# Performance work log

Hardware: AMD Instinct MI355X
Metric: run time of the kernel (lower is better)

The kernel has to match this reference:

```python
import jax, jax.numpy as jnp
import numpy as np

B, T, D, H, E, K = 2, 1024, 1024, 16, 8, 2
HD = D // H
EPS = 1e-5


def _layer_norm(x, g, b):
    m = jnp.mean(x, axis=-1, keepdims=True)
    v = jnp.mean(jnp.square(x - m), axis=-1, keepdims=True)
    return (x - m) * jax.lax.rsqrt(v + EPS) * g + b


def setup_inputs() -> dict:
    key = jax.random.key(0)
    ks = jax.random.split(key, 8)
    s = 0.02
    return {
        "key": jax.random.normal(ks[0], (B, T, D), jnp.float32),
        "ln0_g": jnp.ones((D,), jnp.float32),
        "ln0_b": jnp.zeros((D,), jnp.float32),
        "Wv": s * jax.random.normal(ks[1], (D, D), jnp.float32),
        "Wk": s * jax.random.normal(ks[2], (D, D), jnp.float32),
        "Wq": s * jax.random.normal(ks[3], (D, D), jnp.float32),
        "Wo": s * jax.random.normal(ks[4], (D, D), jnp.float32),
        "ln1_g": jnp.ones((D,), jnp.float32),
        "ln1_b": jnp.zeros((D,), jnp.float32),
        "Wg": s * jax.random.normal(ks[5], (D, E), jnp.float32),
        "bg": jnp.zeros((E,), jnp.float32),
        "W1": s * jax.random.normal(ks[6], (E, D, D), jnp.float32),
        "b1": jnp.zeros((E, D), jnp.float32),
        "W2": s * jax.random.normal(ks[7], (E, D, D), jnp.float32),
        "b2": jnp.zeros((E, D), jnp.float32),
    }


def reference(key, ln0_g, ln0_b, Wv, Wk, Wq, Wo, ln1_g, ln1_b, Wg, bg, W1, b1, W2, b2):
    # pre-norm (shared for q/k/v since query=value=None)
    kn = _layer_norm(key, ln0_g, ln0_b)
    v = (kn @ Wv).reshape(B, T, H, HD)
    k = (kn @ Wk).reshape(B, T, H, HD)
    q = (kn @ Wq).reshape(B, T, H, HD)
    energy = jnp.einsum('bqhd,bkhd->bhqk', q, k)
    # note: source scales by sqrt(input_dim), not sqrt(head_dim)
    attn = jax.nn.softmax(energy / jnp.sqrt(jnp.asarray(D, energy.dtype)), axis=-1)
    o = jnp.einsum('bhqk,bkhd->bqhd', attn, v).reshape(B, T, D) @ Wo
    a = o + key  # residual onto key (query is None)
    xn = _layer_norm(a, ln1_g, ln1_b)
    # --- MoE (top-2 gating, noise_std=0 -> deterministic) ---
    xf = xn.reshape(-1, D)  # [N, D]
    logits = xf @ Wg + bg  # [N, E]
    scores, idx = jax.lax.top_k(logits, K)  # [N, K]
    w = jax.nn.softmax(scores, axis=-1)  # K=2 -> softmax over top-k scores
    # dense dispatch-combine: combine[N,E] = scatter of top-k weights
    combine = jnp.sum(jax.nn.one_hot(idx, E, dtype=xf.dtype) * w[..., None], axis=1)
    h = jax.nn.gelu(jnp.einsum('nd,edh->neh', xf, W1) + b1, approximate=False)
    eo = jnp.einsum('neh,ehf->nef', h, W2) + b2
    moe = jnp.einsum('ne,nef->nf', combine, eo).reshape(B, T, D)
    return moe + a  # out_dim == input_dim -> residual
```

## Files before the change

kernel.cpp:

```cpp
#include <hip/hip_runtime.h>
#include <hip/hip_bf16.h>

#define N_TOK 2048
#define DMODEL 1024
#define NE 8
#define ND (N_TOK * DMODEL)
#define MAT (DMODEL * DMODEL)

typedef __hip_bfloat16 bf16;
typedef __attribute__((ext_vector_type(8))) short s16x8;
typedef __attribute__((ext_vector_type(4))) float f32x4;

__device__ __forceinline__ float b2f(bf16 x) { return __bfloat162float(x); }
__device__ __forceinline__ bf16 f2b(float x) { return __float2bfloat16(x); }

__device__ __forceinline__ bool flag_bf16(const void* ones) {
    return *(const unsigned int*)ones == 0x3F803F80u;
}
__device__ __forceinline__ float ldx(const void* p, size_t i, bool bf) {
    return bf ? __bfloat162float(((const bf16*)p)[i]) : ((const float*)p)[i];
}
__device__ __forceinline__ float gelu_exact(float x) {
    return 0.5f * x * (1.f + erff(x * 0.70710678118654752f));
}

#define GLD16(gp, lp)                                                  \
    __builtin_amdgcn_global_load_lds(                                  \
        (const __attribute__((address_space(1))) void*)(gp),           \
        (__attribute__((address_space(3))) void*)(lp), 16, 0, 0)

#define MFMA16(a, b, c) __builtin_amdgcn_mfma_f32_16x16x32_bf16(a, b, c, 0, 0, 0)

__global__ __launch_bounds__(256) void prep_wT(const void* __restrict__ W,
                                               bf16* __restrict__ o,
                                               const void* __restrict__ ones) {
    bool bf = flag_bf16(ones);
    size_t moff = (size_t)blockIdx.z * MAT;
    int k0 = blockIdx.y * 64, n0 = blockIdx.x * 64;
    __shared__ float t[64][65];
    int tid = threadIdx.x;
#pragma unroll
    for (int i = 0; i < 16; ++i) {
        int idx = tid + 256 * i;
        int r = idx >> 6, c = idx & 63;
        t[r][c] = ldx(W, moff + (size_t)(k0 + r) * DMODEL + n0 + c, bf);
    }
    __syncthreads();
#pragma unroll
    for (int i = 0; i < 16; ++i) {
        int idx = tid + 256 * i;
        int r = idx >> 6, c = idx & 63;
        o[moff + (size_t)(n0 + r) * DMODEL + k0 + c] = f2b(t[c][r]);
    }
}

__global__ __launch_bounds__(256) void prep_wT2(const void* __restrict__ W0,
                                                const void* __restrict__ W1p,
                                                const void* __restrict__ W2p,
                                                bf16* __restrict__ oh,
                                                bf16* __restrict__ ol,
                                                const void* __restrict__ ones) {
    bool bf = flag_bf16(ones);
    int z = blockIdx.z;
    const void* W = (z == 0) ? W0 : (z == 1) ? W1p : W2p;
    size_t moff = (size_t)z * MAT;
    int k0 = blockIdx.y * 64, n0 = blockIdx.x * 64;
    __shared__ float t[64][65];
    int tid = threadIdx.x;
#pragma unroll
    for (int i = 0; i < 16; ++i) {
        int idx = tid + 256 * i;
        int r = idx >> 6, c = idx & 63;
        t[r][c] = ldx(W, (size_t)(k0 + r) * DMODEL + n0 + c, bf);
    }
    __syncthreads();
#pragma unroll
    for (int i = 0; i < 16; ++i) {
        int idx = tid + 256 * i;
        int r = idx >> 6, c = idx & 63;
        float x = t[c][r];
        bf16 hi = f2b(x);
        size_t oi = moff + (size_t)(n0 + r) * DMODEL + k0 + c;
        oh[oi] = hi;
        ol[oi] = f2b(x - b2f(hi));
    }
}

__global__ __launch_bounds__(256) void ln_kernel(const void* __restrict__ in, int in_ext,
                                                 const void* __restrict__ g,
                                                 const void* __restrict__ bb,
                                                 float* __restrict__ out32,
                                                 bf16* __restrict__ outh,
                                                 bf16* __restrict__ outl,
                                                 const void* __restrict__ ones) {
    bool bf = flag_bf16(ones);
    bool inbf = in_ext && bf;
    int row = blockIdx.x, tid = threadIdx.x;
    int lane = tid & 63, wave = tid >> 6;
    float x[4];
#pragma unroll
    for (int i = 0; i < 4; ++i) {
        int idx = tid + 256 * i;
        x[i] = inbf ? b2f(((const bf16*)in)[(size_t)row * DMODEL + idx])
                    : ((const float*)in)[(size_t)row * DMODEL + idx];
    }
    float s = x[0] + x[1] + x[2] + x[3];
    float s2 = x[0] * x[0] + x[1] * x[1] + x[2] * x[2] + x[3] * x[3];
#pragma unroll
    for (int off = 32; off; off >>= 1) {
        s += __shfl_xor(s, off);
        s2 += __shfl_xor(s2, off);
    }
    __shared__ float red[8];
    if (lane == 0) { red[wave] = s; red[4 + wave] = s2; }
    __syncthreads();
    float tot = red[0] + red[1] + red[2] + red[3];
    float tot2 = red[4] + red[5] + red[6] + red[7];
    float m = tot * (1.f / DMODEL);
    float var = tot2 * (1.f / DMODEL) - m * m;
    float rs = rsqrtf(var + 1e-5f);
#pragma unroll
    for (int i = 0; i < 4; ++i) {
        int idx = tid + 256 * i;
        size_t oi = (size_t)row * DMODEL + idx;
        float y = (x[i] - m) * rs * ldx(g, idx, bf) + ldx(bb, idx, bf);
        if (out32) out32[oi] = y;
        if (outh) {
            bf16 hi = f2b(y);
            outh[oi] = hi;
            if (outl) outl[oi] = f2b(y - b2f(hi));
        }
    }
}

template <int MODE>
__global__ __launch_bounds__(256) void split_gemm(const bf16* __restrict__ Ah,
                                                  const bf16* __restrict__ Al,
                                                  const bf16* __restrict__ BTh,
                                                  const bf16* __restrict__ BTl,
                                                  float* __restrict__ Cf,
                                                  const void* __restrict__ resid,
                                                  const void* __restrict__ ones) {
    bool bf = flag_bf16(ones);
    int bx = blockIdx.x, by = blockIdx.y, z = blockIdx.z;
    int m0 = by * 128, n0 = bx * 128;
    BTh += (size_t)z * MAT;
    BTl += (size_t)z * MAT;
    Cf += (size_t)z * ND;

    __shared__ short lds[2][4][128 * 32];
    int tid = threadIdx.x, w = tid >> 6, l = tid & 63;

    size_t aoff[2], boff[2];
#pragma unroll
    for (int i = 0; i < 2; ++i) {
        int tr = w * 32 + i * 16 + (l >> 2);
        aoff[i] = (size_t)(m0 + tr) * (DMODEL * 2) + (size_t)(l & 3) * 16;
        boff[i] = (size_t)(n0 + tr) * (DMODEL * 2) + (size_t)(l & 3) * 16;
    }
    const char* pAh = (const char*)Ah;
    const char* pAl = (const char*)Al;
    const char* pBh = (const char*)BTh;
    const char* pBl = (const char*)BTl;

#pragma unroll
    for (int i = 0; i < 2; ++i) {
        int lb = (w * 32 + i * 16) * 32;
        GLD16(pAh + aoff[i], &lds[0][0][lb]);
        GLD16(pAl + aoff[i], &lds[0][1][lb]);
        GLD16(pBh + boff[i], &lds[0][2][lb]);
        GLD16(pBl + boff[i], &lds[0][3][lb]);
    }

    f32x4 acc[4][4] = {};
    int wm = (w >> 1) * 64, wn = (w & 1) * 64;
    int lrow = l & 15, lk = (l >> 4) * 8;

    for (int kt = 0; kt < 32; ++kt) {
        int cur = kt & 1;
        __syncthreads();
        if (kt < 31) {
            size_t sh = (size_t)(kt + 1) * 64;
#pragma unroll
            for (int i = 0; i < 2; ++i) {
                int lb = (w * 32 + i * 16) * 32;
                GLD16(pAh + sh + aoff[i], &lds[cur ^ 1][0][lb]);
                GLD16(pAl + sh + aoff[i], &lds[cur ^ 1][1][lb]);
                GLD16(pBh + sh + boff[i], &lds[cur ^ 1][2][lb]);
                GLD16(pBl + sh + boff[i], &lds[cur ^ 1][3][lb]);
            }
        }
        s16x8 afh[4], afl[4], bfh[4], bfl[4];
#pragma unroll
        for (int mi = 0; mi < 4; ++mi) {
            afh[mi] = *(const s16x8*)&lds[cur][0][(wm + mi * 16 + lrow) * 32 + lk];
            afl[mi] = *(const s16x8*)&lds[cur][1][(wm + mi * 16 + lrow) * 32 + lk];
        }
#pragma unroll
        for (int ni = 0; ni < 4; ++ni) {
            bfh[ni] = *(const s16x8*)&lds[cur][2][(wn + ni * 16 + lrow) * 32 + lk];
            bfl[ni] = *(const s16x8*)&lds[cur][3][(wn + ni * 16 + lrow) * 32 + lk];
        }
#pragma unroll
        for (int mi = 0; mi < 4; ++mi)
#pragma unroll
            for (int ni = 0; ni < 4; ++ni) {
                acc[mi][ni] = MFMA16(afh[mi], bfh[ni], acc[mi][ni]);
                acc[mi][ni] = MFMA16(afh[mi], bfl[ni], acc[mi][ni]);
                acc[mi][ni] = MFMA16(afl[mi], bfh[ni], acc[mi][ni]);
            }
    }

#pragma unroll
    for (int mi = 0; mi < 4; ++mi)
#pragma unroll
        for (int j = 0; j < 4; ++j) {
            size_t p = (size_t)(m0 + wm + mi * 16 + (l >> 4) * 4 + j);
#pragma unroll
            for (int ni = 0; ni < 4; ++ni) {
                int col = n0 + wn + ni * 16 + lrow;
                float v = acc[mi][ni][j];
                if (MODE == 1) v += ldx(resid, p * DMODEL + col, bf);
                Cf[p * DMODEL + col] = v;
            }
        }
}

template <int MODE>
__global__ __launch_bounds__(256) void moe_gemm(const bf16* __restrict__ A,
                                                const bf16* __restrict__ BT,
                                                bf16* __restrict__ Cb,
                                                const void* __restrict__ bias,
                                                const int* __restrict__ cnt,
                                                const int* __restrict__ lists,
                                                const float* __restrict__ wts,
                                                const void* __restrict__ ones) {
    bool bf = flag_bf16(ones);
    int bx = blockIdx.x, by = blockIdx.y, z = blockIdx.z;
    int count = cnt[z];
    lists += z * N_TOK;
    int m0 = by * 128, n0 = bx * 128;
    if (m0 >= count) return;
    BT += (size_t)z * MAT;
    size_t biasoff = (size_t)z * DMODEL;

    __shared__ short lds[2][2][128 * 32];
    int tid = threadIdx.x, w = tid >> 6, l = tid & 63;

    size_t aoff[2], boff[2];
#pragma unroll
    for (int i = 0; i < 2; ++i) {
        int tr = w * 32 + i * 16 + (l >> 2);
        int p = m0 + tr;
        if (p >= count) p = count - 1;
        int aid = lists[p];
        size_t arow = (MODE == 2) ? (size_t)(aid >> 1) : (size_t)aid;
        aoff[i] = arow * (DMODEL * 2) + (size_t)(l & 3) * 16;
        boff[i] = (size_t)(n0 + tr) * (DMODEL * 2) + (size_t)(l & 3) * 16;
    }
    const char* Ab = (const char*)A;
    const char* Bb = (const char*)BT;

#pragma unroll
    for (int i = 0; i < 2; ++i) {
        int lb = (w * 32 + i * 16) * 32;
        GLD16(Ab + aoff[i], &lds[0][0][lb]);
        GLD16(Bb + boff[i], &lds[0][1][lb]);
    }

    f32x4 acc[4][4] = {};
    int wm = (w >> 1) * 64, wn = (w & 1) * 64;
    int lrow = l & 15, lk = (l >> 4) * 8;

    for (int kt = 0; kt < 32; ++kt) {
        int cur = kt & 1;
        __syncthreads();
        if (kt < 31) {
            size_t sh = (size_t)(kt + 1) * 64;
#pragma unroll
            for (int i = 0; i < 2; ++i) {
                int lb = (w * 32 + i * 16) * 32;
                GLD16(Ab + sh + aoff[i], &lds[cur ^ 1][0][lb]);
                GLD16(Bb + sh + boff[i], &lds[cur ^ 1][1][lb]);
            }
        }
        s16x8 af[4], bfr[4];
#pragma unroll
        for (int mi = 0; mi < 4; ++mi)
            af[mi] = *(const s16x8*)&lds[cur][0][(wm + mi * 16 + lrow) * 32 + lk];
#pragma unroll
        for (int ni = 0; ni < 4; ++ni)
            bfr[ni] = *(const s16x8*)&lds[cur][1][(wn + ni * 16 + lrow) * 32 + lk];
#pragma unroll
        for (int mi = 0; mi < 4; ++mi)
#pragma unroll
            for (int ni = 0; ni < 4; ++ni) acc[mi][ni] = MFMA16(af[mi], bfr[ni], acc[mi][ni]);
    }

#pragma unroll
    for (int mi = 0; mi < 4; ++mi)
#pragma unroll
        for (int j = 0; j < 4; ++j) {
            int p = m0 + wm + mi * 16 + (l >> 4) * 4 + j;
            if (p >= count) continue;
            int aid = lists[p];
            float wgt = (MODE == 3) ? wts[aid] : 1.f;
#pragma unroll
            for (int ni = 0; ni < 4; ++ni) {
                int col = n0 + wn + ni * 16 + lrow;
                float v = acc[mi][ni][j];
                if (MODE == 2)
                    Cb[(size_t)aid * DMODEL + col] =
                        f2b(gelu_exact(v + ldx(bias, biasoff + col, bf)));
                else
                    Cb[(size_t)aid * DMODEL + col] = f2b(wgt * (v + ldx(bias, biasoff + col, bf)));
            }
        }
}

__global__ __launch_bounds__(256) void attn_kernel(const float* __restrict__ q,
                                                   const float* __restrict__ k,
                                                   const float* __restrict__ v,
                                                   bf16* __restrict__ oh,
                                                   bf16* __restrict__ ol) {
    const int b = blockIdx.z, h = blockIdx.y, q0 = blockIdx.x * 8;
    __shared__ float S[8][1024];
    __shared__ float Qs[8][64];
    int tid = threadIdx.x;
    const size_t base = ((size_t)b * 1024) * DMODEL + h * 64;
#pragma unroll
    for (int i = 0; i < 2; ++i) {
        int idx = tid + 256 * i;
        int qi = idx >> 6, d = idx & 63;
        Qs[qi][d] = q[base + (size_t)(q0 + qi) * DMODEL + d];
    }
    __syncthreads();
    const float scale = 0.03125f;
    for (int kk = tid; kk < 1024; kk += 256) {
        const float* kr = &k[base + (size_t)kk * DMODEL];
        float acc[8] = {};
        for (int d = 0; d < 64; ++d) {
            float kv = kr[d];
#pragma unroll
            for (int qi = 0; qi < 8; ++qi) acc[qi] += kv * Qs[qi][d];
        }
#pragma unroll
        for (int qi = 0; qi < 8; ++qi) S[qi][kk] = acc[qi] * scale;
    }
    __syncthreads();
    int wave = tid >> 6, lane = tid & 63;
    for (int qi = wave; qi < 8; qi += 4) {
        float m = -1e30f;
        for (int kk = lane; kk < 1024; kk += 64) m = fmaxf(m, S[qi][kk]);
#pragma unroll
        for (int off = 32; off; off >>= 1) m = fmaxf(m, __shfl_xor(m, off));
        float ssum = 0.f;
        for (int kk = lane; kk < 1024; kk += 64) {
            float p = expf(S[qi][kk] - m);
            S[qi][kk] = p;
            ssum += p;
        }
#pragma unroll
        for (int off = 32; off; off >>= 1) ssum += __shfl_xor(ssum, off);
        float inv = 1.f / ssum;
        for (int kk = lane; kk < 1024; kk += 64) S[qi][kk] *= inv;
    }
    __syncthreads();
    int d = tid & 63, part = tid >> 6;
    float acc[8] = {};
    for (int kk = part * 256; kk < part * 256 + 256; ++kk) {
        float vv = v[base + (size_t)kk * DMODEL + d];
#pragma unroll
        for (int qi = 0; qi < 8; ++qi) acc[qi] += S[qi][kk] * vv;
    }
    __syncthreads();
    float* red = &S[0][0];
#pragma unroll
    for (int qi = 0; qi < 8; ++qi) red[(part * 8 + qi) * 64 + d] = acc[qi];
    __syncthreads();
    if (part == 0) {
#pragma unroll
        for (int qi = 0; qi < 8; ++qi) {
            float s = red[(0 * 8 + qi) * 64 + d] + red[(1 * 8 + qi) * 64 + d] +
                      red[(2 * 8 + qi) * 64 + d] + red[(3 * 8 + qi) * 64 + d];
            size_t oi = base + (size_t)(q0 + qi) * DMODEL + d;
            bf16 hi = f2b(s);
            oh[oi] = hi;
            ol[oi] = f2b(s - b2f(hi));
        }
    }
}

__global__ __launch_bounds__(256) void gate_kernel(const float* __restrict__ xn,
                                                   const void* __restrict__ Wg,
                                                   const void* __restrict__ bg,
                                                   int* __restrict__ cnt,
                                                   int* __restrict__ lists,
                                                   float* __restrict__ wts,
                                                   const void* __restrict__ ones) {
    bool bf = flag_bf16(ones);
    int wave = threadIdx.x >> 6, lane = threadIdx.x & 63;
    int n = blockIdx.x * 4 + wave;
    const float* xr = xn + (size_t)n * DMODEL;
    float s[NE] = {};
    for (int i = lane; i < DMODEL; i += 64) {
        float xv = xr[i];
#pragma unroll
        for (int e = 0; e < NE; ++e) s[e] += xv * ldx(Wg, (size_t)i * NE + e, bf);
    }
#pragma unroll
    for (int e = 0; e < NE; ++e)
#pragma unroll
        for (int off = 32; off; off >>= 1) s[e] += __shfl_xor(s[e], off);
    if (lane == 0) {
#pragma unroll
        for (int e = 0; e < NE; ++e) s[e] += ldx(bg, e, bf);
        int b0 = 0;
#pragma unroll
        for (int e = 1; e < NE; ++e)
            if (s[e] > s[b0]) b0 = e;
        int b1 = (b0 == 0) ? 1 : 0;
#pragma unroll
        for (int e = 0; e < NE; ++e)
            if (e != b0 && s[e] > s[b1]) b1 = e;
        float w0 = 1.f / (1.f + expf(s[b1] - s[b0]));
        float w1 = 1.f - w0;
        int p0 = atomicAdd(&cnt[b0], 1);
        lists[b0 * N_TOK + p0] = (n << 1);
        int p1 = atomicAdd(&cnt[b1], 1);
        lists[b1 * N_TOK + p1] = (n << 1) | 1;
        wts[2 * n] = w0;
        wts[2 * n + 1] = w1;
    }
}

__global__ __launch_bounds__(256) void combine_kernel(const bf16* __restrict__ eo,
                                                      const float* __restrict__ a,
                                                      void* __restrict__ out,
                                                      const void* __restrict__ ones) {
    bool bf = flag_bf16(ones);
    int i = blockIdx.x * 256 + threadIdx.x;
    int n = i >> 10, d = i & 1023;
    float v = b2f(eo[((size_t)(2 * n)) * DMODEL + d]) +
              b2f(eo[((size_t)(2 * n + 1)) * DMODEL + d]) + a[i];
    if (bf)
        ((bf16*)out)[i] = f2b(v);
    else
        ((float*)out)[i] = v;
}

extern "C" void kernel_launch(void* const* d_in, const int* in_sizes, int n_in,
                              void* d_out, int out_size, void* d_ws, size_t ws_size,
                              hipStream_t stream) {
    const void* key = d_in[0];
    const void* ln0g = d_in[1];
    const void* ln0b = d_in[2];
    const void* Wv = d_in[3];
    const void* Wk = d_in[4];
    const void* Wq = d_in[5];
    const void* Wo = d_in[6];
    const void* ln1g = d_in[7];
    const void* ln1b = d_in[8];
    const void* Wg = d_in[9];
    const void* bg = d_in[10];
    const void* W1 = d_in[11];
    const void* b1 = d_in[12];
    const void* W2 = d_in[13];
    const void* b2 = d_in[14];

    char* W = (char*)d_ws;
    bf16* wQh = (bf16*)W;
    bf16* wQl = (bf16*)(W + (6u << 20));
    bf16* knh = (bf16*)(W + (12u << 20));
    bf16* knl = (bf16*)(W + (16u << 20));
    float* qkv = (float*)(W + (20u << 20));
    bf16* oh = knh;
    bf16* ol = knl;
    bf16* wOh = (bf16*)W;
    bf16* wOl = (bf16*)(W + (2u << 20));
    float* ab = qkv;
    float* xn32 = (float*)(W + (28u << 20));
    bf16* xnb = (bf16*)(W + (36u << 20));
    bf16* wE = (bf16*)W;
    bf16* hbuf = (bf16*)(W + (40u << 20));
    bf16* eo = (bf16*)(W + (28u << 20));
    int* cnt = (int*)(W + (48u << 20));
    int* lists = cnt + 16;
    float* wts = (float*)(lists + NE * N_TOK);

    ln_kernel<<<N_TOK, 256, 0, stream>>>(key, 1, ln0g, ln0b, nullptr, knh, knl, ln0g);

    prep_wT2<<<dim3(16, 16, 3), 256, 0, stream>>>(Wv, Wk, Wq, wQh, wQl, ln0g);
    split_gemm<0><<<dim3(8, 16, 3), 256, 0, stream>>>(knh, knl, wQh, wQl, qkv, nullptr, ln0g);

    attn_kernel<<<dim3(128, 16, 2), 256, 0, stream>>>(qkv + 2 * (size_t)ND, qkv + ND, qkv, oh, ol);

    prep_wT2<<<dim3(16, 16, 1), 256, 0, stream>>>(Wo, nullptr, nullptr, wOh, wOl, ln0g);
    split_gemm<1><<<dim3(8, 16, 1), 256, 0, stream>>>(oh, ol, wOh, wOl, ab, key, ln0g);

    ln_kernel<<<N_TOK, 256, 0, stream>>>(ab, 0, ln1g, ln1b, xn32, xnb, nullptr, ln0g);

    hipMemsetAsync(cnt, 0, 16 * sizeof(int), stream);
    gate_kernel<<<N_TOK / 4, 256, 0, stream>>>(xn32, Wg, bg, cnt, lists, wts, ln0g);

    prep_wT<<<dim3(16, 16, 8), 256, 0, stream>>>(W1, wE, ln0g);
    moe_gemm<2><<<dim3(8, 16, 8), 256, 0, stream>>>(xnb, wE, hbuf, b1, cnt, lists, wts, ln0g);
    prep_wT<<<dim3(16, 16, 8), 256, 0, stream>>>(W2, wE, ln0g);
    moe_gemm<3><<<dim3(8, 16, 8), 256, 0, stream>>>(hbuf, wE, eo, b2, cnt, lists, wts, ln0g);

    combine_kernel<<<ND / 256, 256, 0, stream>>>(eo, ab, d_out, ln0g);
}
```

Measured before the change: 534.3 us.

## Use split-bf16 MFMA for attention QK and PV with bf16 QKV outputs

The QKV projection GEMM now writes hi/lo bf16 pairs directly, with V stored transposed, instead of fp32. The attention kernel replaces its scalar fp32 QK^T and PV loops with 16x16x32 bf16 MFMA using three-product split precision. The score buffer gets a padded row stride to reduce LDS bank conflicts. This targets the scalar-FMA-bound attention kernel, at the cost of approximate fp32 via bf16 splitting and strided transposed stores for V.

```diff
diff --git a/kernel.cpp b/kernel.cpp
--- a/kernel.cpp
+++ b/kernel.cpp
@@ -6,6 +6,7 @@
 #define NE 8
 #define ND (N_TOK * DMODEL)
 #define MAT (DMODEL * DMODEL)
+#define SS 1032
 
 typedef __hip_bfloat16 bf16;
 typedef __attribute__((ext_vector_type(8))) short s16x8;
@@ -13,6 +14,7 @@
 
 __device__ __forceinline__ float b2f(bf16 x) { return __bfloat162float(x); }
 __device__ __forceinline__ bf16 f2b(float x) { return __float2bfloat16(x); }
+__device__ __forceinline__ short bbits(bf16 x) { return __builtin_bit_cast(short, x); }
 
 __device__ __forceinline__ bool flag_bf16(const void* ones) {
     return *(const unsigned int*)ones == 0x3F803F80u;
@@ -139,6 +141,8 @@
                                                   const bf16* __restrict__ BTh,
                                                   const bf16* __restrict__ BTl,
                                                   float* __restrict__ Cf,
+                                                  bf16* __restrict__ Cbh,
+                                                  bf16* __restrict__ Cbl,
                                                   const void* __restrict__ resid,
                                                   const void* __restrict__ ones) {
     bool bf = flag_bf16(ones);
@@ -146,7 +150,11 @@
     int m0 = by * 128, n0 = bx * 128;
     BTh += (size_t)z * MAT;
     BTl += (size_t)z * MAT;
-    Cf += (size_t)z * ND;
+    if (MODE == 0) {
+        Cbh += (size_t)z * ND;
+        Cbl += (size_t)z * ND;
+    }
+    if (MODE == 1) Cf += (size_t)z * ND;
 
     __shared__ short lds[2][4][128 * 32];
     int tid = threadIdx.x, w = tid >> 6, l = tid & 63;
@@ -220,8 +228,17 @@
             for (int ni = 0; ni < 4; ++ni) {
                 int col = n0 + wn + ni * 16 + lrow;
                 float v = acc[mi][ni][j];
-                if (MODE == 1) v += ldx(resid, p * DMODEL + col, bf);
-                Cf[p * DMODEL + col] = v;
+                if (MODE == 0) {
+                    bf16 hi = f2b(v);
+                    Cbh[p * DMODEL + col] = hi;
+                    Cbl[p * DMODEL + col] = f2b(v - b2f(hi));
+                } else if (MODE == 1) {
+                    Cf[p * DMODEL + col] = v + ldx(resid, p * DMODEL + col, bf);
+                } else {
+                    bf16 hi = f2b(v);
+                    Cbh[(size_t)col * N_TOK + p] = hi;
+                    Cbl[(size_t)col * N_TOK + p] = f2b(v - b2f(hi));
+                }
             }
         }
 }
@@ -318,75 +335,97 @@
         }
 }
 
-__global__ __launch_bounds__(256) void attn_kernel(const float* __restrict__ q,
-                                                   const float* __restrict__ k,
-                                                   const float* __restrict__ v,
-                                                   bf16* __restrict__ oh,
-                                                   bf16* __restrict__ ol) {
+__global__ __launch_bounds__(256) void attn_qkpv(const bf16* __restrict__ qh,
+                                                 const bf16* __restrict__ ql,
+                                                 const bf16* __restrict__ kh,
+                                                 const bf16* __restrict__ kl,
+                                                 const bf16* __restrict__ vth,
+                                                 const bf16* __restrict__ vtl,
+                                                 bf16* __restrict__ oh,
+                                                 bf16* __restrict__ ol) {
     const int b = blockIdx.z, h = blockIdx.y, q0 = blockIdx.x * 8;
-    __shared__ float S[8][1024];
-    __shared__ float Qs[8][64];
-    int tid = threadIdx.x;
-    const size_t base = ((size_t)b * 1024) * DMODEL + h * 64;
-#pragma unroll
-    for (int i = 0; i < 2; ++i) {
-        int idx = tid + 256 * i;
-        int qi = idx >> 6, d = idx & 63;
-        Qs[qi][d] = q[base + (size_t)(q0 + qi) * DMODEL + d];
+    __shared__ float S[8 * SS];
+    int tid = threadIdx.x, w = tid >> 6, l = tid & 63;
+    int lr = l & 15, lg = l >> 4;
+
+    s16x8 qfh[2], qfl[2];
+    {
+        size_t qrow = ((size_t)(b << 10) + q0 + (lr & 7)) * DMODEL + h * 64 + lg * 8;
+#pragma unroll
+        for (int ks = 0; ks < 2; ++ks) {
+            qfh[ks] = *(const s16x8*)(qh + qrow + ks * 32);
+            qfl[ks] = *(const s16x8*)(ql + qrow + ks * 32);
+        }
+    }
+    const float scale = 0.03125f;
+
+#pragma unroll 2
+    for (int kf = 0; kf < 16; ++kf) {
+        f32x4 s = {0.f, 0.f, 0.f, 0.f};
+        size_t krow = ((size_t)(b << 10) + w * 256 + kf * 16 + lr) * DMODEL + h * 64 + lg * 8;
+#pragma unroll
+        for (int ks = 0; ks < 2; ++ks) {
+            s16x8 bh = *(const s16x8*)(kh + krow + ks * 32);
+            s16x8 bl = *(const s16x8*)(kl + krow + ks * 32);
+            s = MFMA16(qfh[ks], bh, s);
+            s = MFMA16(qfh[ks], bl, s);
+            s = MFMA16(qfl[ks], bh, s);
+        }
+        if (lg < 2) {
+#pragma unroll
+            for (int j = 0; j < 4; ++j) S[(lg * 4 + j) * SS + w * 256 + kf * 16 + lr] = s[j] * scale;
+        }
     }
     __syncthreads();
-    const float scale = 0.03125f;
-    for (int kk = tid; kk < 1024; kk += 256) {
-        const float* kr = &k[base + (size_t)kk * DMODEL];
-        float acc[8] = {};
-        for (int d = 0; d < 64; ++d) {
-            float kv = kr[d];
-#pragma unroll
-            for (int qi = 0; qi < 8; ++qi) acc[qi] += kv * Qs[qi][d];
-        }
-#pragma unroll
-        for (int qi = 0; qi < 8; ++qi) S[qi][kk] = acc[qi] * scale;
-    }
-    __syncthreads();
+
     int wave = tid >> 6, lane = tid & 63;
     for (int qi = wave; qi < 8; qi += 4) {
         float m = -1e30f;
-        for (int kk = lane; kk < 1024; kk += 64) m = fmaxf(m, S[qi][kk]);
+        for (int kk = lane; kk < 1024; kk += 64) m = fmaxf(m, S[qi * SS + kk]);
 #pragma unroll
         for (int off = 32; off; off >>= 1) m = fmaxf(m, __shfl_xor(m, off));
         float ssum = 0.f;
         for (int kk = lane; kk < 1024; kk += 64) {
-            float p = expf(S[qi][kk] - m);
-            S[qi][kk] = p;
+            float p = expf(S[qi * SS + kk] - m);
+            S[qi * SS + kk] = p;
             ssum += p;
         }
 #pragma unroll
         for (int off = 32; off; off >>= 1) ssum += __shfl_xor(ssum, off);
         float inv = 1.f / ssum;
-        for (int kk = lane; kk < 1024; kk += 64) S[qi][kk] *= inv;
+        for (int kk = lane; kk < 1024; kk += 64) S[qi * SS + kk] *= inv;
     }
     __syncthreads();
-    int d = tid & 63, part = tid >> 6;
-    float acc[8] = {};
-    for (int kk = part * 256; kk < part * 256 + 256; ++kk) {
-        float vv = v[base + (size_t)kk * DMODEL + d];
-#pragma unroll
-        for (int qi = 0; qi < 8; ++qi) acc[qi] += S[qi][kk] * vv;
-    }
-    __syncthreads();
-    float* red = &S[0][0];
-#pragma unroll
-    for (int qi = 0; qi < 8; ++qi) red[(part * 8 + qi) * 64 + d] = acc[qi];
-    __syncthreads();
-    if (part == 0) {
-#pragma unroll
-        for (int qi = 0; qi < 8; ++qi) {
-            float s = red[(0 * 8 + qi) * 64 + d] + red[(1 * 8 + qi) * 64 + d] +
-                      red[(2 * 8 + qi) * 64 + d] + red[(3 * 8 + qi) * 64 + d];
-            size_t oi = base + (size_t)(q0 + qi) * DMODEL + d;
-            bf16 hi = f2b(s);
+
+    f32x4 oacc = {0.f, 0.f, 0.f, 0.f};
+    size_t vrow = ((size_t)(h * 64) + w * 16 + lr) * (size_t)N_TOK + ((size_t)b << 10);
+#pragma unroll 2
+    for (int c = 0; c < 32; ++c) {
+        f32x4 p0 = *(const f32x4*)&S[(lr & 7) * SS + c * 32 + lg * 8];
+        f32x4 p1 = *(const f32x4*)&S[(lr & 7) * SS + c * 32 + lg * 8 + 4];
+        s16x8 pah, pal;
+#pragma unroll
+        for (int i = 0; i < 4; ++i) {
+            bf16 h0 = f2b(p0[i]), h1 = f2b(p1[i]);
+            pah[i] = bbits(h0);
+            pah[4 + i] = bbits(h1);
+            pal[i] = bbits(f2b(p0[i] - b2f(h0)));
+            pal[4 + i] = bbits(f2b(p1[i] - b2f(h1)));
+        }
+        s16x8 vbh = *(const s16x8*)(vth + vrow + c * 32 + lg * 8);
+        s16x8 vbl = *(const s16x8*)(vtl + vrow + c * 32 + lg * 8);
+        oacc = MFMA16(pah, vbh, oacc);
+        oacc = MFMA16(pah, vbl, oacc);
+        oacc = MFMA16(pal, vbh, oacc);
+    }
+    if (lg < 2) {
+#pragma unroll
+        for (int j = 0; j < 4; ++j) {
+            float o = oacc[j];
+            size_t oi = ((size_t)(b << 10) + q0 + lg * 4 + j) * DMODEL + h * 64 + w * 16 + lr;
+            bf16 hi = f2b(o);
             oh[oi] = hi;
-            ol[oi] = f2b(s - b2f(hi));
+            ol[oi] = f2b(o - b2f(hi));
         }
     }
 }
@@ -473,12 +512,17 @@
     bf16* wQl = (bf16*)(W + (6u << 20));
     bf16* knh = (bf16*)(W + (12u << 20));
     bf16* knl = (bf16*)(W + (16u << 20));
-    float* qkv = (float*)(W + (20u << 20));
+    bf16* vTh = (bf16*)(W + (20u << 20));
+    bf16* kh = (bf16*)(W + (24u << 20));
+    bf16* qh = (bf16*)(W + (28u << 20));
+    bf16* vTl = (bf16*)(W + (32u << 20));
+    bf16* kl = (bf16*)(W + (36u << 20));
+    bf16* ql = (bf16*)(W + (40u << 20));
     bf16* oh = knh;
     bf16* ol = knl;
     bf16* wOh = (bf16*)W;
     bf16* wOl = (bf16*)(W + (2u << 20));
-    float* ab = qkv;
+    float* ab = (float*)(W + (20u << 20));
     float* xn32 = (float*)(W + (28u << 20));
     bf16* xnb = (bf16*)(W + (36u << 20));
     bf16* wE = (bf16*)W;
@@ -491,12 +535,16 @@
     ln_kernel<<<N_TOK, 256, 0, stream>>>(key, 1, ln0g, ln0b, nullptr, knh, knl, ln0g);
 
     prep_wT2<<<dim3(16, 16, 3), 256, 0, stream>>>(Wv, Wk, Wq, wQh, wQl, ln0g);
-    split_gemm<0><<<dim3(8, 16, 3), 256, 0, stream>>>(knh, knl, wQh, wQl, qkv, nullptr, ln0g);
-
-    attn_kernel<<<dim3(128, 16, 2), 256, 0, stream>>>(qkv + 2 * (size_t)ND, qkv + ND, qkv, oh, ol);
+    split_gemm<2><<<dim3(8, 16, 1), 256, 0, stream>>>(knh, knl, wQh, wQl, nullptr, vTh, vTl,
+                                                      nullptr, ln0g);
+    split_gemm<0><<<dim3(8, 16, 2), 256, 0, stream>>>(knh, knl, wQh + MAT, wQl + MAT, nullptr, kh,
+                                                      kl, nullptr, ln0g);
+
+    attn_qkpv<<<dim3(128, 16, 2), 256, 0, stream>>>(qh, ql, kh, kl, vTh, vTl, oh, ol);
 
     prep_wT2<<<dim3(16, 16, 1), 256, 0, stream>>>(Wo, nullptr, nullptr, wOh, wOl, ln0g);
-    split_gemm<1><<<dim3(8, 16, 1), 256, 0, stream>>>(oh, ol, wOh, wOl, ab, key, ln0g);
+    split_gemm<1><<<dim3(8, 16, 1), 256, 0, stream>>>(oh, ol, wOh, wOl, ab, nullptr, nullptr, key,
+                                                      ln0g);
 
     ln_kernel<<<N_TOK, 256, 0, stream>>>(ab, 0, ln1g, ln1b, xn32, xnb, nullptr, ln0g);
 
```

New measurement: 576.7 us. +8.0%, slower.
